# Kernel optimization log

Measured on AMD Instinct MI355X. Metric: run time of the kernel, lower is better.

The kernel has to match this reference:

```python
import jax, jax.numpy as jnp
import numpy as np

EPS = 1e-4          # eps in build_deterministic_repr
TEMPERING = 0.1     # self.tempering
GUMBEL_TEMP = 0.1   # temperature in sample_gumbel_softmax
GUMBEL_EPS = 1e-8


def _conv1d(x, w, b, stride=2):
    # x: (N, Cin, L), w: (Cout, Cin, K)  -> valid conv, stride 2 (matches nn.Conv1d)
    y = jax.lax.conv_general_dilated(x, w, window_strides=(stride,), padding='VALID',
                                     dimension_numbers=('NCH', 'OIH', 'NCH'))
    return y + b[None, :, None]


def setup_inputs() -> dict:
    key = jax.random.key(0)
    ks = jax.random.split(key, 12)
    nb, G, C, ch, nmix, hdim, ns = 8, 2048, 512, 8, 4, 10, 10
    xc = jax.random.uniform(ks[0], (nb, C, 1, ch), minval=-2.0, maxval=2.0)
    yc = jax.random.normal(ks[1], (nb, C, ch))
    # xgrid is a linspace over the data range (build_xgrid), broadcast to all dims/channels
    xgrid = jnp.broadcast_to(jnp.linspace(-3.0, 3.0, G)[None, :, None, None],
                             (nb, G, 1, ch)).astype(jnp.float32)
    log_ls = 0.1 * jax.random.normal(ks[2], (ch,))
    w1 = 0.1 * jax.random.normal(ks[3], (hdim, ch, 5));  b1 = jnp.zeros((hdim,))
    w2 = 0.1 * jax.random.normal(ks[4], (hdim, hdim, 5)); b2 = jnp.zeros((hdim,))
    w3 = 0.1 * jax.random.normal(ks[5], (hdim, hdim, 5)); b3 = jnp.zeros((hdim,))
    w4 = 0.1 * jax.random.normal(ks[6], (hdim, hdim, 5)); b4 = jnp.zeros((hdim,))
    wl = 0.1 * jax.random.normal(ks[7], (nmix * ch, hdim)); bl = jnp.zeros((nmix * ch,))
    unif = jax.random.uniform(ks[8], (nb, ns, ch, nmix), minval=1e-6, maxval=1.0)
    return dict(xc=xc, yc=yc, xgrid=xgrid, log_ls=log_ls,
                w1=w1, b1=b1, w2=w2, b2=b2, w3=w3, b3=b3, w4=w4, b4=b4,
                wl=wl, bl=bl, unif=unif)


def reference(xc, yc, xgrid, log_ls, w1, b1, w2, b2, w3, b3, w4, b4, wl, bl, unif):
    nb, G, _, ch = xgrid.shape
    ls = jnp.exp(log_ls)                                    # per-channel RBF lengthscale
    # ---- build_deterministic_repr: RBF Kxt + density / weighted datarepr ----
    # d2[b,g,c,H] = sum_dim (xgrid - xc)^2
    d2 = ((xgrid[:, :, None, :, :] - xc[:, None, :, :, :]) ** 2).sum(axis=3)  # (nb,G,C,ch)
    K = jnp.exp(-0.5 * d2 / (ls ** 2))                      # (nb,G,C,ch)
    density = K.sum(axis=2)                                 # (nb,G,ch)
    datarepr = jnp.einsum('bgcH,bcH->bgH', K, yc) / (density + EPS)  # (nb,G,ch)
    # ---- build_mixweight: weight net on detached datarepr ----
    x = jnp.transpose(jax.lax.stop_gradient(datarepr), (0, 2, 1))   # (nb,ch,G)
    h = jax.nn.relu(_conv1d(x, w1, b1))
    h = jax.nn.relu(_conv1d(h, w2, b2))
    h = jax.nn.relu(_conv1d(h, w3, b3))
    h = _conv1d(h, w4, b4)
    h = h.mean(axis=-1)                                     # AdaptiveAvgPool1d(1)
    logit = h @ wl.T + bl                                   # (nb, nmix*ch)
    logit = logit.reshape(nb, ch, -1)                       # (nb,ch,nmix)
    logit = (logit - logit.max(axis=-1, keepdims=True)) / TEMPERING
    mixweight = jax.nn.softmax(logit, axis=-1)
    # ---- sample_gumbel_softmax on the tempered logits ----
    g = -jnp.log(-jnp.log(unif + GUMBEL_EPS))               # (nb,ns,ch,nmix)
    hh = (g + logit[:, None, :, :]) / GUMBEL_TEMP
    y = jax.nn.softmax(hh - hh.max(axis=-1, keepdims=True), axis=-1)
    mixweight_sample = jnp.clip(y, GUMBEL_EPS, 1.0 - GUMBEL_EPS)
    return density, datarepr, mixweight, mixweight_sample
```

## Files before the change

kernel.cpp:

```cpp
#include <hip/hip_runtime.h>
#include <hip/hip_bf16.h>

#define NB 8
#define G  2048
#define C  512
#define CH 8
#define NM 4
#define HD 10
#define NS 10
#define L1 1022
#define L2 509
#define L3 253
#define L4 125

__global__ __launch_bounds__(256) void k_density(
    const float* __restrict__ xc, const float* __restrict__ yc,
    const float* __restrict__ xg, const float* __restrict__ logls,
    float* __restrict__ out_den,
    float* __restrict__ out_rep)
{
    __shared__ float2 sxy[C];
    __shared__ float sden[4][64];
    __shared__ float snum[4][64];
    const int tid  = threadIdx.x;
    const int lane = tid & 63;
    const int wv   = tid >> 6;
    const int id = blockIdx.x;
    const int gt = id & 31;
    const int H  = (id >> 5) & 7;
    const int b  = id >> 8;

    for (int c = tid; c < C; c += 256)
        sxy[c] = make_float2(xc[(b * C + c) * CH + H], yc[(b * C + c) * CH + H]);
    __syncthreads();

    const int g = gt * 64 + lane;
    const float x = xg[(b * G + g) * CH + H];
    const float coef = -0.72134752044448170f * __expf(-2.0f * logls[H]);

    const float2* p = sxy + wv * 128;
    float den = 0.0f, num = 0.0f;
    #pragma unroll 8
    for (int c = 0; c < 128; ++c) {
        const float2 v = p[c];
        const float d = x - v.x;
        const float w = __builtin_amdgcn_exp2f((d * coef) * d);
        den += w;
        num = fmaf(w, v.y, num);
    }

    sden[wv][lane] = den;
    snum[wv][lane] = num;
    __syncthreads();

    if (tid < 64) {
        const float dtot = sden[0][tid] + sden[1][tid] + sden[2][tid] + sden[3][tid];
        const float ntot = snum[0][tid] + snum[1][tid] + snum[2][tid] + snum[3][tid];
        const int o = (b * G + gt * 64 + tid) * CH + H;
        out_den[o] = dtot;
        out_rep[o] = ntot / (dtot + 1e-4f);
    }
}

__global__ __launch_bounds__(256) void k_convnet(
    const float* __restrict__ rep,
    const float* __restrict__ w1, const float* __restrict__ b1,
    const float* __restrict__ w2, const float* __restrict__ b2,
    const float* __restrict__ w3, const float* __restrict__ b3,
    const float* __restrict__ w4, const float* __restrict__ b4,
    float* __restrict__ h4out)
{
    const int b   = blockIdx.x / 25;
    const int t   = blockIdx.x % 25;
    const int tid = threadIdx.x;

    __shared__ float sxt[CH * 125];
    __shared__ float sw1[5 * CH * HD];
    __shared__ float sw2[5 * HD * HD];
    __shared__ float sw3[5 * HD * HD];
    __shared__ float sw4[5 * HD * HD];
    __shared__ float s1[HD * 61];
    __shared__ float s2[HD * 29];
    __shared__ float s3[HD * 13];

    {
        const float* src = rep + (b * G + 80 * t) * CH;
        for (int i = tid; i < 125 * CH; i += 256) {
            const int gl = i >> 3, ci = i & 7;
            sxt[ci * 125 + gl] = src[i];
        }
    }
    for (int i = tid; i < HD * CH * 5; i += 256) {
        const int o = i / 40, ci = (i / 5) % 8, k = i % 5;
        sw1[(k * CH + ci) * HD + o] = w1[i];
    }
    for (int i = tid; i < HD * HD * 5; i += 256) {
        const int o = i / 50, ci = (i / 5) % 10, k = i % 5;
        sw2[(k * HD + ci) * HD + o] = w2[i];
        sw3[(k * HD + ci) * HD + o] = w3[i];
        sw4[(k * HD + ci) * HD + o] = w4[i];
    }
    __syncthreads();

    for (int i = tid; i < 61 * HD; i += 256) {
        const int o = i % HD, ll = i / HD;
        float acc = b1[o];
        #pragma unroll
        for (int k = 0; k < 5; ++k)
            #pragma unroll
            for (int ci = 0; ci < CH; ++ci)
                acc = fmaf(sxt[ci * 125 + 2 * ll + k], sw1[(k * CH + ci) * HD + o], acc);
        s1[o * 61 + ll] = fmaxf(acc, 0.0f);
    }
    __syncthreads();

    for (int i = tid; i < 29 * HD; i += 256) {
        const int o = i % HD, ll = i / HD;
        float acc = b2[o];
        #pragma unroll
        for (int k = 0; k < 5; ++k)
            #pragma unroll
            for (int ci = 0; ci < HD; ++ci)
                acc = fmaf(s1[ci * 61 + 2 * ll + k], sw2[(k * HD + ci) * HD + o], acc);
        s2[o * 29 + ll] = fmaxf(acc, 0.0f);
    }
    __syncthreads();

    for (int i = tid; i < 13 * HD; i += 256) {
        const int o = i % HD, ll = i / HD;
        float acc = b3[o];
        #pragma unroll
        for (int k = 0; k < 5; ++k)
            #pragma unroll
            for (int ci = 0; ci < HD; ++ci)
                acc = fmaf(s2[ci * 29 + 2 * ll + k], sw3[(k * HD + ci) * HD + o], acc);
        s3[o * 13 + ll] = fmaxf(acc, 0.0f);
    }
    __syncthreads();

    for (int i = tid; i < 5 * HD; i += 256) {
        const int o = i % HD, ll = i / HD;
        float acc = b4[o];
        #pragma unroll
        for (int k = 0; k < 5; ++k)
            #pragma unroll
            for (int ci = 0; ci < HD; ++ci)
                acc = fmaf(s3[ci * 13 + 2 * ll + k], sw4[(k * HD + ci) * HD + o], acc);
        h4out[(b * HD + o) * L4 + 5 * t + ll] = acc;
    }
}

__global__ __launch_bounds__(256) void k_tail(
    const float* __restrict__ h4,
    const float* __restrict__ wl, const float* __restrict__ bl,
    const float* __restrict__ unif,
    float* __restrict__ out_mw,
    float* __restrict__ out_ms)
{
    const int b   = blockIdx.x;
    const int tid = threadIdx.x;
    __shared__ float red[HD * 25];
    __shared__ float hm[HD];
    __shared__ float lg[CH * NM];
    __shared__ float ltt[CH * NM];

    if (tid < HD * 25) {
        const int o = tid / 25, j = tid % 25;
        const float* p = h4 + (b * HD + o) * L4 + j * 5;
        red[tid] = p[0] + p[1] + p[2] + p[3] + p[4];
    }
    __syncthreads();
    if (tid < HD) {
        float s = 0.0f;
        #pragma unroll
        for (int j = 0; j < 25; ++j) s += red[tid * 25 + j];
        hm[tid] = s * (1.0f / (float)L4);
    }
    __syncthreads();
    if (tid < CH * NM) {
        float acc = bl[tid];
        #pragma unroll
        for (int k = 0; k < HD; ++k) acc = fmaf(wl[tid * HD + k], hm[k], acc);
        lg[tid] = acc;
    }
    __syncthreads();
    if (tid < CH) {
        float lv[NM];
        #pragma unroll
        for (int m = 0; m < NM; ++m) lv[m] = lg[tid * NM + m];
        const float m0 = fmaxf(fmaxf(lv[0], lv[1]), fmaxf(lv[2], lv[3]));
        float e[NM], s = 0.0f;
        #pragma unroll
        for (int m = 0; m < NM; ++m) {
            const float v = (lv[m] - m0) / 0.1f;
            ltt[tid * NM + m] = v;
            e[m] = __expf(v);
            s += e[m];
        }
        #pragma unroll
        for (int m = 0; m < NM; ++m)
            out_mw[(b * CH + tid) * NM + m] = e[m] / s;
    }
    __syncthreads();
    if (tid < NS * CH) {
        const int c = tid % CH, sI = tid / CH;
        const float* up = unif + ((b * NS + sI) * CH + c) * NM;
        float hh[NM], mx = -1e30f;
        #pragma unroll
        for (int m = 0; m < NM; ++m) {
            const float gu = -__logf(-__logf(up[m] + 1e-8f));
            hh[m] = (gu + ltt[c * NM + m]) / 0.1f;
            mx = fmaxf(mx, hh[m]);
        }
        float e2[NM], ss = 0.0f;
        #pragma unroll
        for (int m = 0; m < NM; ++m) { e2[m] = __expf(hh[m] - mx); ss += e2[m]; }
        #pragma unroll
        for (int m = 0; m < NM; ++m) {
            float y = e2[m] / ss;
            y = fminf(fmaxf(y, 1e-8f), 1.0f - 1e-8f);
            out_ms[((b * NS + sI) * CH + c) * NM + m] = y;
        }
    }
}

extern "C" void kernel_launch(void* const* d_in, const int* in_sizes, int n_in,
                              void* d_out, int out_size, void* d_ws, size_t ws_size,
                              hipStream_t stream) {
    const float* xc    = (const float*)d_in[0];
    const float* yc    = (const float*)d_in[1];
    const float* xg    = (const float*)d_in[2];
    const float* logls = (const float*)d_in[3];
    const float* w1    = (const float*)d_in[4];
    const float* b1    = (const float*)d_in[5];
    const float* w2    = (const float*)d_in[6];
    const float* b2    = (const float*)d_in[7];
    const float* w3    = (const float*)d_in[8];
    const float* b3    = (const float*)d_in[9];
    const float* w4    = (const float*)d_in[10];
    const float* b4    = (const float*)d_in[11];
    const float* wl    = (const float*)d_in[12];
    const float* bl    = (const float*)d_in[13];
    const float* unif  = (const float*)d_in[14];

    float* out = (float*)d_out;
    float* out_den = out;
    float* out_rep = out + NB * G * CH;
    float* out_mw  = out + 2 * NB * G * CH;
    float* out_ms  = out_mw + NB * CH * NM;
    (void)out_size; (void)in_sizes; (void)n_in; (void)ws_size;

    float* ws_h4 = (float*)d_ws;

    k_density<<<2048, 256, 0, stream>>>(xc, yc, xg, logls, out_den, out_rep);

    k_convnet<<<NB * 25, 256, 0, stream>>>(out_rep, w1, b1, w2, b2, w3, b3, w4, b4,
                                           ws_h4);

    k_tail<<<NB, 256, 0, stream>>>(ws_h4, wl, bl, unif, out_mw, out_ms);
}
```

Baseline: 28.95 us.

## Factor RBF exponent and fold tail into convnet via last-block counter

The density loop now expands (x - xc)^2 so that each iteration is a single fma feeding exp2. The x-only factor exp2(coef*x^2) is applied once after the reduction, and coef*xc^2 is precomputed into a float4 in shared memory. The separate tail kernel is removed: each convnet block increments a per-batch atomic counter, and the last block for that batch runs the mean pool, linear, softmax and gumbel stages. The counter is reset inside the density kernel. This removes one launch and trims ALU work in the hot loop, in exchange for some rounding error from the expanded exponent, wider shared-memory reads, and a threadfence/atomic handshake.

```diff
diff --git a/kernel.cpp b/kernel.cpp
--- a/kernel.cpp
+++ b/kernel.cpp
@@ -17,9 +17,10 @@
     const float* __restrict__ xc, const float* __restrict__ yc,
     const float* __restrict__ xg, const float* __restrict__ logls,
     float* __restrict__ out_den,
-    float* __restrict__ out_rep)
+    float* __restrict__ out_rep,
+    int* __restrict__ cnt)
 {
-    __shared__ float2 sxy[C];
+    __shared__ __align__(16) float4 sxyq[C];
     __shared__ float sden[4][64];
     __shared__ float snum[4][64];
     const int tid  = threadIdx.x;
@@ -30,23 +31,31 @@
     const int H  = (id >> 5) & 7;
     const int b  = id >> 8;
 
-    for (int c = tid; c < C; c += 256)
-        sxy[c] = make_float2(xc[(b * C + c) * CH + H], yc[(b * C + c) * CH + H]);
+    if (id == 0 && tid < NB) cnt[tid] = 0;
+
+    const float coef = -0.72134752044448170f * __expf(-2.0f * logls[H]);
+
+    for (int c = tid; c < C; c += 256) {
+        const float xx = xc[(b * C + c) * CH + H];
+        const float yy = yc[(b * C + c) * CH + H];
+        sxyq[c] = make_float4(xx, yy, coef * xx * xx, 0.0f);
+    }
     __syncthreads();
 
     const int g = gt * 64 + lane;
     const float x = xg[(b * G + g) * CH + H];
-    const float coef = -0.72134752044448170f * __expf(-2.0f * logls[H]);
-
-    const float2* p = sxy + wv * 128;
+    const float A = coef * x * x;
+    const float B = -2.0f * coef * x;
+    const float EA = __builtin_amdgcn_exp2f(A);
+
+    const float4* p = sxyq + wv * 128;
     float den = 0.0f, num = 0.0f;
     #pragma unroll 8
     for (int c = 0; c < 128; ++c) {
-        const float2 v = p[c];
-        const float d = x - v.x;
-        const float w = __builtin_amdgcn_exp2f((d * coef) * d);
-        den += w;
-        num = fmaf(w, v.y, num);
+        const float4 v = p[c];
+        const float e = __builtin_amdgcn_exp2f(fmaf(B, v.x, v.z));
+        den += e;
+        num = fmaf(e, v.y, num);
     }
 
     sden[wv][lane] = den;
@@ -56,9 +65,10 @@
     if (tid < 64) {
         const float dtot = sden[0][tid] + sden[1][tid] + sden[2][tid] + sden[3][tid];
         const float ntot = snum[0][tid] + snum[1][tid] + snum[2][tid] + snum[3][tid];
+        const float denf = EA * dtot;
         const int o = (b * G + gt * 64 + tid) * CH + H;
-        out_den[o] = dtot;
-        out_rep[o] = ntot / (dtot + 1e-4f);
+        out_den[o] = denf;
+        out_rep[o] = (EA * ntot) / (denf + 1e-4f);
     }
 }
 
@@ -68,7 +78,12 @@
     const float* __restrict__ w2, const float* __restrict__ b2,
     const float* __restrict__ w3, const float* __restrict__ b3,
     const float* __restrict__ w4, const float* __restrict__ b4,
-    float* __restrict__ h4out)
+    const float* __restrict__ wl, const float* __restrict__ bl,
+    const float* __restrict__ unif,
+    float* __restrict__ h4out,
+    int* __restrict__ cnt,
+    float* __restrict__ out_mw,
+    float* __restrict__ out_ms)
 {
     const int b   = blockIdx.x / 25;
     const int t   = blockIdx.x % 25;
@@ -82,6 +97,11 @@
     __shared__ float s1[HD * 61];
     __shared__ float s2[HD * 29];
     __shared__ float s3[HD * 13];
+    __shared__ float red[HD * 25];
+    __shared__ float hm[HD];
+    __shared__ float lg[CH * NM];
+    __shared__ float ltt[CH * NM];
+    __shared__ int   do_tail;
 
     {
         const float* src = rep + (b * G + 80 * t) * CH;
@@ -148,26 +168,21 @@
                 acc = fmaf(s3[ci * 13 + 2 * ll + k], sw4[(k * HD + ci) * HD + o], acc);
         h4out[(b * HD + o) * L4 + 5 * t + ll] = acc;
     }
-}
-
-__global__ __launch_bounds__(256) void k_tail(
-    const float* __restrict__ h4,
-    const float* __restrict__ wl, const float* __restrict__ bl,
-    const float* __restrict__ unif,
-    float* __restrict__ out_mw,
-    float* __restrict__ out_ms)
-{
-    const int b   = blockIdx.x;
-    const int tid = threadIdx.x;
-    __shared__ float red[HD * 25];
-    __shared__ float hm[HD];
-    __shared__ float lg[CH * NM];
-    __shared__ float ltt[CH * NM];
-
+
+    __syncthreads();
+    if (tid == 0) {
+        __threadfence();
+        do_tail = (atomicAdd(&cnt[b], 1) == 24) ? 1 : 0;
+    }
+    __syncthreads();
+    if (!do_tail) return;
+    __threadfence();
+
+    const volatile float* h4 = h4out;
     if (tid < HD * 25) {
         const int o = tid / 25, j = tid % 25;
-        const float* p = h4 + (b * HD + o) * L4 + j * 5;
-        red[tid] = p[0] + p[1] + p[2] + p[3] + p[4];
+        const int base = (b * HD + o) * L4 + j * 5;
+        red[tid] = h4[base] + h4[base + 1] + h4[base + 2] + h4[base + 3] + h4[base + 4];
     }
     __syncthreads();
     if (tid < HD) {
@@ -251,11 +266,10 @@
     (void)out_size; (void)in_sizes; (void)n_in; (void)ws_size;
 
     float* ws_h4 = (float*)d_ws;
-
-    k_density<<<2048, 256, 0, stream>>>(xc, yc, xg, logls, out_den, out_rep);
+    int*   cnt   = (int*)(ws_h4 + NB * HD * L4);
+
+    k_density<<<2048, 256, 0, stream>>>(xc, yc, xg, logls, out_den, out_rep, cnt);
 
     k_convnet<<<NB * 25, 256, 0, stream>>>(out_rep, w1, b1, w2, b2, w3, b3, w4, b4,
-                                           ws_h4);
-
-    k_tail<<<NB, 256, 0, stream>>>(ws_h4, wl, bl, unif, out_mw, out_ms);
+                                           wl, bl, unif, ws_h4, cnt, out_mw, out_ms);
 }
```

Measured after the change: 39.52 us. +36.5%, slower.

## Fuse tail kernel into convnet kernel using per-batch atomic completion counters

Applied to the files above, without the earlier changes.

Removes the third kernel launch by appending NB extra blocks to the convnet grid. These blocks spin-wait on a per-batch atomic counter until all 25 conv tiles for their batch have finished, then run the mean-pool, linear, softmax and Gumbel-softmax tail. The density kernel resets the counters. This trades a launch boundary for in-kernel spinning, which risks deadlock if the tail blocks occupy resources before the producer blocks are scheduled, and it adds fence and atomic overhead.

```diff
diff --git a/kernel.cpp b/kernel.cpp
--- a/kernel.cpp
+++ b/kernel.cpp
@@ -17,7 +17,8 @@
     const float* __restrict__ xc, const float* __restrict__ yc,
     const float* __restrict__ xg, const float* __restrict__ logls,
     float* __restrict__ out_den,
-    float* __restrict__ out_rep)
+    float* __restrict__ out_rep,
+    int* __restrict__ cnt)
 {
     __shared__ float2 sxy[C];
     __shared__ float sden[4][64];
@@ -30,6 +31,8 @@
     const int H  = (id >> 5) & 7;
     const int b  = id >> 8;
 
+    if (id == 0 && tid < NB) cnt[tid] = 0;
+
     for (int c = tid; c < C; c += 256)
         sxy[c] = make_float2(xc[(b * C + c) * CH + H], yc[(b * C + c) * CH + H]);
     __syncthreads();
@@ -68,11 +71,93 @@
     const float* __restrict__ w2, const float* __restrict__ b2,
     const float* __restrict__ w3, const float* __restrict__ b3,
     const float* __restrict__ w4, const float* __restrict__ b4,
-    float* __restrict__ h4out)
+    const float* __restrict__ wl, const float* __restrict__ bl,
+    const float* __restrict__ unif,
+    float* __restrict__ h4out,
+    int* __restrict__ cnt,
+    float* __restrict__ out_mw,
+    float* __restrict__ out_ms)
 {
-    const int b   = blockIdx.x / 25;
-    const int t   = blockIdx.x % 25;
     const int tid = threadIdx.x;
+
+    if (blockIdx.x >= NB * 25) {
+        const int b = blockIdx.x - NB * 25;
+        __shared__ float red[HD * 25];
+        __shared__ float hm[HD];
+        __shared__ float lg[CH * NM];
+        __shared__ float ltt[CH * NM];
+
+        if (tid == 0) {
+            while (__hip_atomic_load(&cnt[b], __ATOMIC_RELAXED,
+                                     __HIP_MEMORY_SCOPE_AGENT) < 25)
+                __builtin_amdgcn_s_sleep(16);
+        }
+        __syncthreads();
+        __threadfence();
+
+        if (tid < HD * 25) {
+            const int o = tid / 25, j = tid % 25;
+            const float* p = h4out + (b * HD + o) * L4 + j * 5;
+            red[tid] = p[0] + p[1] + p[2] + p[3] + p[4];
+        }
+        __syncthreads();
+        if (tid < HD) {
+            float s = 0.0f;
+            #pragma unroll
+            for (int j = 0; j < 25; ++j) s += red[tid * 25 + j];
+            hm[tid] = s * (1.0f / (float)L4);
+        }
+        __syncthreads();
+        if (tid < CH * NM) {
+            float acc = bl[tid];
+            #pragma unroll
+            for (int k = 0; k < HD; ++k) acc = fmaf(wl[tid * HD + k], hm[k], acc);
+            lg[tid] = acc;
+        }
+        __syncthreads();
+        if (tid < CH) {
+            float lv[NM];
+            #pragma unroll
+            for (int m = 0; m < NM; ++m) lv[m] = lg[tid * NM + m];
+            const float m0 = fmaxf(fmaxf(lv[0], lv[1]), fmaxf(lv[2], lv[3]));
+            float e[NM], s = 0.0f;
+            #pragma unroll
+            for (int m = 0; m < NM; ++m) {
+                const float v = (lv[m] - m0) / 0.1f;
+                ltt[tid * NM + m] = v;
+                e[m] = __expf(v);
+                s += e[m];
+            }
+            #pragma unroll
+            for (int m = 0; m < NM; ++m)
+                out_mw[(b * CH + tid) * NM + m] = e[m] / s;
+        }
+        __syncthreads();
+        if (tid < NS * CH) {
+            const int c = tid % CH, sI = tid / CH;
+            const float* up = unif + ((b * NS + sI) * CH + c) * NM;
+            float hh[NM], mx = -1e30f;
+            #pragma unroll
+            for (int m = 0; m < NM; ++m) {
+                const float gu = -__logf(-__logf(up[m] + 1e-8f));
+                hh[m] = (gu + ltt[c * NM + m]) / 0.1f;
+                mx = fmaxf(mx, hh[m]);
+            }
+            float e2[NM], ss = 0.0f;
+            #pragma unroll
+            for (int m = 0; m < NM; ++m) { e2[m] = __expf(hh[m] - mx); ss += e2[m]; }
+            #pragma unroll
+            for (int m = 0; m < NM; ++m) {
+                float y = e2[m] / ss;
+                y = fminf(fmaxf(y, 1e-8f), 1.0f - 1e-8f);
+                out_ms[((b * NS + sI) * CH + c) * NM + m] = y;
+            }
+        }
+        return;
+    }
+
+    const int b = blockIdx.x / 25;
+    const int t = blockIdx.x % 25;
 
     __shared__ float sxt[CH * 125];
     __shared__ float sw1[5 * CH * HD];
@@ -148,79 +233,11 @@
                 acc = fmaf(s3[ci * 13 + 2 * ll + k], sw4[(k * HD + ci) * HD + o], acc);
         h4out[(b * HD + o) * L4 + 5 * t + ll] = acc;
     }
-}
-
-__global__ __launch_bounds__(256) void k_tail(
-    const float* __restrict__ h4,
-    const float* __restrict__ wl, const float* __restrict__ bl,
-    const float* __restrict__ unif,
-    float* __restrict__ out_mw,
-    float* __restrict__ out_ms)
-{
-    const int b   = blockIdx.x;
-    const int tid = threadIdx.x;
-    __shared__ float red[HD * 25];
-    __shared__ float hm[HD];
-    __shared__ float lg[CH * NM];
-    __shared__ float ltt[CH * NM];
-
-    if (tid < HD * 25) {
-        const int o = tid / 25, j = tid % 25;
-        const float* p = h4 + (b * HD + o) * L4 + j * 5;
-        red[tid] = p[0] + p[1] + p[2] + p[3] + p[4];
-    }
-    __syncthreads();
-    if (tid < HD) {
-        float s = 0.0f;
-        #pragma unroll
-        for (int j = 0; j < 25; ++j) s += red[tid * 25 + j];
-        hm[tid] = s * (1.0f / (float)L4);
-    }
-    __syncthreads();
-    if (tid < CH * NM) {
-        float acc = bl[tid];
-        #pragma unroll
-        for (int k = 0; k < HD; ++k) acc = fmaf(wl[tid * HD + k], hm[k], acc);
-        lg[tid] = acc;
-    }
-    __syncthreads();
-    if (tid < CH) {
-        float lv[NM];
-        #pragma unroll
-        for (int m = 0; m < NM; ++m) lv[m] = lg[tid * NM + m];
-        const float m0 = fmaxf(fmaxf(lv[0], lv[1]), fmaxf(lv[2], lv[3]));
-        float e[NM], s = 0.0f;
-        #pragma unroll
-        for (int m = 0; m < NM; ++m) {
-            const float v = (lv[m] - m0) / 0.1f;
-            ltt[tid * NM + m] = v;
-            e[m] = __expf(v);
-            s += e[m];
-        }
-        #pragma unroll
-        for (int m = 0; m < NM; ++m)
-            out_mw[(b * CH + tid) * NM + m] = e[m] / s;
-    }
-    __syncthreads();
-    if (tid < NS * CH) {
-        const int c = tid % CH, sI = tid / CH;
-        const float* up = unif + ((b * NS + sI) * CH + c) * NM;
-        float hh[NM], mx = -1e30f;
-        #pragma unroll
-        for (int m = 0; m < NM; ++m) {
-            const float gu = -__logf(-__logf(up[m] + 1e-8f));
-            hh[m] = (gu + ltt[c * NM + m]) / 0.1f;
-            mx = fmaxf(mx, hh[m]);
-        }
-        float e2[NM], ss = 0.0f;
-        #pragma unroll
-        for (int m = 0; m < NM; ++m) { e2[m] = __expf(hh[m] - mx); ss += e2[m]; }
-        #pragma unroll
-        for (int m = 0; m < NM; ++m) {
-            float y = e2[m] / ss;
-            y = fminf(fmaxf(y, 1e-8f), 1.0f - 1e-8f);
-            out_ms[((b * NS + sI) * CH + c) * NM + m] = y;
-        }
+
+    __syncthreads();
+    if (tid == 0) {
+        __threadfence();
+        atomicAdd(&cnt[b], 1);
     }
 }
 
@@ -251,11 +268,11 @@
     (void)out_size; (void)in_sizes; (void)n_in; (void)ws_size;
 
     float* ws_h4 = (float*)d_ws;
-
-    k_density<<<2048, 256, 0, stream>>>(xc, yc, xg, logls, out_den, out_rep);
-
-    k_convnet<<<NB * 25, 256, 0, stream>>>(out_rep, w1, b1, w2, b2, w3, b3, w4, b4,
-                                           ws_h4);
-
-    k_tail<<<NB, 256, 0, stream>>>(ws_h4, wl, bl, unif, out_mw, out_ms);
+    int*   cnt   = (int*)(ws_h4 + NB * HD * L4);
+
+    k_density<<<2048, 256, 0, stream>>>(xc, yc, xg, logls, out_den, out_rep, cnt);
+
+    k_convnet<<<NB * 25 + NB, 256, 0, stream>>>(out_rep, w1, b1, w2, b2, w3, b3,
+                                                w4, b4, wl, bl, unif,
+                                                ws_h4, cnt, out_mw, out_ms);
 }
```

After: 36.02 us. 1.24x slower.
